# Optimization experiments

Hardware: AMD Instinct MI355X
Metric: run time of the kernel (lower is better)

Reference implementation:

```python
import jax, jax.numpy as jnp
from jax import lax
import numpy as np

B = 8; T = 64000
NFFT = 1024; HOP = 256
SC = 20; KS = 1024; PAD = 512
HEADS = 8; GH = 64; GO = 32
SPEC_DIM = 32 * (NFFT // 4) // 2   # 4096
NODE_DIM = SC + SPEC_DIM           # 4116
EPS = 1e-5
NEG_SLOPE = 0.2


def setup_inputs() -> dict:
    ks = jax.random.split(jax.random.key(0), 12)
    f32 = jnp.float32
    def rn(k, shp, s):
        return jax.random.normal(k, shp, dtype=f32) * s
    return {
        "x": jax.random.normal(ks[0], (B, 1, T), dtype=f32),
        "sinc_w": rn(ks[1], (SC, 1, KS), 0.03),
        "conv1_w": rn(ks[2], (32, 1, 3, 3), 0.1),
        "conv1_b": jnp.zeros((32,), f32),
        "bn1_g": jnp.ones((32,), f32),
        "bn1_b": jnp.zeros((32,), f32),
        "conv2_w": rn(ks[3], (32, 32, 3, 3), 0.06),
        "conv2_b": jnp.zeros((32,), f32),
        "bn2_g": jnp.ones((32,), f32),
        "bn2_b": jnp.zeros((32,), f32),
        "gat1_W": rn(ks[4], (NODE_DIM, HEADS * GH), 0.015),
        "gat1_asrc": rn(ks[5], (HEADS, GH), 0.1),
        "gat1_adst": rn(ks[6], (HEADS, GH), 0.1),
        "gat1_bias": jnp.zeros((HEADS * GH,), f32),
        "gat2_W": rn(ks[7], (HEADS * GH, GO), 0.04),
        "gat2_asrc": rn(ks[8], (1, GO), 0.1),
        "gat2_adst": rn(ks[9], (1, GO), 0.1),
        "gat2_bias": jnp.zeros((GO,), f32),
        "fc1_w": rn(ks[10], (GO, 128), 0.15),
        "fc1_b": jnp.zeros((128,), f32),
        "bnf_g": jnp.ones((128,), f32),
        "bnf_b": jnp.zeros((128,), f32),
        "fc2_w": rn(ks[11], (128, 2), 0.08),
        "fc2_b": jnp.zeros((2,), f32),
    }


def _bn2d_eval(z, g, b):
    # eval-mode BatchNorm2d with running_mean=0, running_var=1
    s = g / jnp.sqrt(1.0 + EPS)
    return z * s[None, :, None, None] + b[None, :, None, None]


def _conv2d(z, w, b):
    y = lax.conv_general_dilated(z, w, (1, 1), ((1, 1), (1, 1)),
                                 dimension_numbers=("NCHW", "OIHW", "NCHW"))
    return y + b[None, :, None, None]


def _gat_dense(hin, W, asrc, adst, bias, heads, fo, concat):
    # PyG GATConv on a fully-connected graph (add_self_loops=True default
    # => every node attends to all nodes including itself). Eval mode (no dropout).
    b, n, d = hin.shape
    h = jnp.einsum("bnd,dhf->bnhf", hin, W.reshape(d, heads, fo))
    s_src = jnp.einsum("bnhf,hf->bnh", h, asrc)   # alpha_j contribution
    s_dst = jnp.einsum("bnhf,hf->bnh", h, adst)   # alpha_i contribution
    e = jax.nn.leaky_relu(s_dst[:, :, None, :] + s_src[:, None, :, :], NEG_SLOPE)  # (b,i,j,h)
    a = jax.nn.softmax(e, axis=2)                 # softmax over sources j per dest i
    out = jnp.einsum("bijh,bjhf->bihf", a, h)
    out = out.reshape(b, n, heads * fo) if concat else out.mean(axis=2)
    return out + bias


def reference(x, sinc_w, conv1_w, conv1_b, bn1_g, bn1_b, conv2_w, conv2_b,
              bn2_g, bn2_b, gat1_W, gat1_asrc, gat1_adst, gat1_bias,
              gat2_W, gat2_asrc, gat2_adst, gat2_bias,
              fc1_w, fc1_b, bnf_g, bnf_b, fc2_w, fc2_b):
    b = x.shape[0]
    # --- sinc (band-pass) conv branch: conv1d k=1024, pad=512 ---
    sinc = lax.conv_general_dilated(x, sinc_w, (1,), ((PAD, PAD),),
                                    dimension_numbers=("NCH", "OIH", "NCH"))  # (b,20,T+1)
    Ls = (sinc.shape[-1] // 4) * 4
    sinc_feat = sinc[:, :, :Ls].reshape(b, SC, Ls // 4, 4).mean(-1)  # avg_pool1d(4)
    sinc_feat = jnp.transpose(sinc_feat, (0, 2, 1))                  # (b, Ls//4, 20)

    # --- STFT branch (torch.stft: center=True, reflect pad, rect window) ---
    xw = x[:, 0, :]
    xp = jnp.pad(xw, ((0, 0), (NFFT // 2, NFFT // 2)), mode="reflect")
    n_frames = 1 + T // HOP  # 251
    idx = np.arange(n_frames)[:, None] * HOP + np.arange(NFFT)
    frames = xp[:, idx]                                   # (b, 251, 1024)
    mag = jnp.abs(jnp.fft.rfft(frames, axis=-1))          # (b, 251, 513)
    logmag = jnp.log(mag + 1e-9)
    s = jnp.transpose(logmag, (0, 2, 1))[:, None]         # (b, 1, 513, 251)

    h = jax.nn.relu(_bn2d_eval(_conv2d(s, conv1_w, conv1_b), bn1_g, bn1_b))
    h = jax.nn.relu(_bn2d_eval(_conv2d(h, conv2_w, conv2_b), bn2_g, bn2_b))
    Fq = (h.shape[2] // 2) * 2
    Tt = (h.shape[3] // 2) * 2
    h = h[:, :, :Fq, :Tt].reshape(b, 32, Fq // 2, 2, Tt // 2, 2).max(axis=(3, 5))  # maxpool 2x2
    spec_feat = jnp.transpose(h, (0, 3, 1, 2)).reshape(b, -1, SPEC_DIM)  # (b, 250, 4096)

    n = min(sinc_feat.shape[1], spec_feat.shape[1])  # 250
    nodes = jnp.concatenate([sinc_feat[:, :n], spec_feat[:, :n]], axis=-1)  # (b,250,4116)

    g1 = jax.nn.relu(_gat_dense(nodes, gat1_W, gat1_asrc, gat1_adst, gat1_bias, HEADS, GH, True))
    g2 = _gat_dense(g1, gat2_W, gat2_asrc, gat2_adst, gat2_bias, 1, GO, False)
    emb = g2.mean(axis=1)  # (b, 32) graph-mean readout

    z = emb @ fc1_w + fc1_b
    z = jax.nn.relu(z * (bnf_g / jnp.sqrt(1.0 + EPS)) + bnf_b)  # eval BN1d
    out = z @ fc2_w + fc2_b
    return (out, emb)
```

## Files before the change

kernel.cpp:

```cpp
#include <hip/hip_runtime.h>
#include <hip/hip_bf16.h>
#include <math.h>

#define TB 8
#define TT 64000
#define NFRAMES 251
#define NROWS (TB*NFRAMES)
#define GROWS 2048
#define NBINS 513
#define NBPAD 576
#define NNODE 250
#define NODE_DIM 4116
#define KPAD 4128

typedef __attribute__((ext_vector_type(8))) short short8;
typedef __attribute__((ext_vector_type(4))) float floatx4;

static __device__ __forceinline__ unsigned short f2bf(float x) {
    __hip_bfloat16 h = __float2bfloat16(x);
    return *(unsigned short*)&h;
}
static __device__ __forceinline__ float bf2f(unsigned short u) {
    __hip_bfloat16 h = *(__hip_bfloat16*)&u;
    return __bfloat162float(h);
}

__global__ __launch_bounds__(256) void k_prep(
    const float* __restrict__ x, const float* __restrict__ sinc_w,
    const float* __restrict__ c2w, const float* __restrict__ g2bn,
    const float* __restrict__ c1w, const float* __restrict__ g1bn,
    const float* __restrict__ W,
    unsigned short* __restrict__ fh, unsigned short* __restrict__ fl,
    unsigned short* __restrict__ bch, unsigned short* __restrict__ bcl,
    unsigned short* __restrict__ bsh, unsigned short* __restrict__ bsl,
    unsigned short* __restrict__ wbt, unsigned short* __restrict__ Bp,
    unsigned short* __restrict__ Bc1,
    unsigned short* __restrict__ Wt, unsigned short* __restrict__ nodesb,
    unsigned short* __restrict__ h1t, unsigned short* __restrict__ h2t) {
    __shared__ unsigned short tile[64][65];
    int bi = blockIdx.x, tid = threadIdx.x;
    if (bi < 2048) {
        int idx = bi * 256 + tid;
        int row = idx >> 8, r = idx & 255;
        int b = row >> 8, j = row & 255;
        int u = j * 256 + r - 512;
        if (u < 0) u = -u;
        if (u >= TT) u = 2 * TT - 2 - u;
        float v = x[b * TT + u];
        unsigned short h = f2bf(v);
        fh[idx] = h;
        fl[idx] = f2bf(v - bf2f(h));
    } else if (bi < 2624) {
        int idx = (bi - 2048) * 256 + tid;
        int k = idx >> 8, r = idx & 255;
        float s = 0.f, c = 0.f;
        if (k < NBINS) {
            int mm = (k * r) & 1023;
            sincospif((float)mm * (1.0f / 512.0f), &s, &c);
        }
        unsigned short chv = f2bf(c), shv = f2bf(s);
        bch[idx] = chv; bcl[idx] = f2bf(c - bf2f(chv));
        bsh[idx] = shv; bsl[idx] = f2bf(s - bf2f(shv));
    } else if (bi < 3144) {
        int local = bi - 2624;
        int kt = local % 65, nt = local / 65;
        for (int idx = tid; idx < 4096; idx += 256) {
            int r = idx >> 6, c = idx & 63;
            int kp = kt * 64 + r;
            int k;
            if (kp < 20) k = kp;
            else if (kp < NODE_DIM) { int t = kp - 20; k = 20 + (t & 15) * 256 + (t >> 4); }
            else k = -1;
            float v = (k >= 0) ? W[k * 512 + nt * 64 + c] : 0.f;
            tile[r][c] = f2bf(v);
        }
        __syncthreads();
        for (int idx = tid; idx < 4096; idx += 256) {
            int nl = idx >> 6, kl = idx & 63;
            int k = kt * 64 + kl;
            if (k < KPAD)
                Wt[(size_t)(nt * 64 + nl) * KPAD + k] = tile[kl][nl];
        }
    } else if (bi < 3276) {
        int idx = (bi - 3144) * 256 + tid;
        if (idx < 32 * 1056) {
            int c = idx / 1056, m = idx - c * 1056;
            float s = 0.f;
            if (c < 20 && m < 1027) {
                #pragma unroll
                for (int d = 0; d < 4; d++) {
                    int k = m - d;
                    if (k >= 0 && k < 1024) s += sinc_w[c * 1024 + k];
                }
                s *= 0.25f;
            }
            wbt[idx] = f2bf(s);
        }
    } else if (bi < 3312) {
        int idx = (bi - 3276) * 256 + tid;
        if (idx < 9216) {
            int j = idx & 7, lane = (idx >> 3) & 63, ct = (idx >> 9) & 1, s = idx >> 10;
            int co = ct * 16 + (lane & 15);
            int ci = (lane >> 4) * 8 + j;
            float inv = rsqrtf(1.0f + 1e-5f);
            Bp[idx] = f2bf(c2w[co * 288 + ci * 9 + s] * (g2bn[co] * inv));
        }
    } else if (bi < 3508) {
        int idx = (bi - 3312) * 256 + tid;
        if (idx < 24000) {
            int row = idx / 12, c = idx - row * 12;
            nodesb[(size_t)row * KPAD + 4116 + c] = 0;
        } else if (idx < 48576) {
            int t = idx - 24000; int r = t / 6, c = t - r * 6;
            h1t[(size_t)r * 256 + 250 + c] = 0;
        } else if (idx < 50112) {
            int t = idx - 48576; int r = t / 6, c = t - r * 6;
            h2t[(size_t)r * 256 + 250 + c] = 0;
        }
    } else {
        int idx = (bi - 3508) * 256 + tid;
        if (idx < 1024) {
            int ch = idx >> 5, k = idx & 31;
            float inv = rsqrtf(1.0f + 1e-5f);
            int t; int typ;
            if (k < 8)       { t = k;      typ = 0; }
            else if (k < 16) { t = k - 8;  typ = 0; }
            else if (k < 24) { t = k - 16; typ = 1; }
            else if (k == 24 || k == 25) { t = 8; typ = 0; }
            else if (k == 26) { t = 8; typ = 1; }
            else { t = 0; typ = 2; }
            unsigned short outv = 0;
            if (typ != 2) {
                float wv = c1w[ch * 9 + t] * (g1bn[ch] * inv);
                unsigned short whi = f2bf(wv);
                outv = (typ == 0) ? whi : f2bf(wv - bf2f(whi));
            }
            Bc1[idx] = outv;
        }
    }
}

__global__ __launch_bounds__(256) void k_sincm(const float* __restrict__ x,
                                               const unsigned short* __restrict__ wbt,
                                               unsigned short* __restrict__ nodesb) {
    __shared__ __align__(16) unsigned short xs[1312];
    int ut = blockIdx.x, b = blockIdx.y;
    int tid = threadIdx.x;
    int base = 256 * ut - 512;
    for (int i = tid; i < 1312; i += 256) {
        int g = base + i;
        float v = (g >= 0 && g < TT) ? x[b * TT + g] : 0.f;
        xs[i] = f2bf(v);
    }
    __syncthreads();
    int w = tid >> 6, lane = tid & 63;
    int q = lane >> 4, col = lane & 15;
    floatx4 acc[2];
    acc[0] = acc[1] = (floatx4){0.f, 0.f, 0.f, 0.f};
    for (int K0 = 0; K0 < 1056; K0 += 32) {
        int off = 4 * (w * 16 + col) + K0 + q * 8;
        unsigned long long lo = *(const unsigned long long*)&xs[off];
        unsigned long long hi = *(const unsigned long long*)&xs[off + 4];
        union { unsigned long long u64[2]; short8 s8; } cv;
        cv.u64[0] = lo; cv.u64[1] = hi;
        short8 af = cv.s8;
        #pragma unroll
        for (int ni = 0; ni < 2; ni++) {
            short8 bf = *(const short8*)(wbt + (size_t)(ni * 16 + col) * 1056 + K0 + q * 8);
            acc[ni] = __builtin_amdgcn_mfma_f32_16x16x32_bf16(af, bf, acc[ni], 0, 0, 0);
        }
    }
    #pragma unroll
    for (int ni = 0; ni < 2; ni++)
        #pragma unroll
        for (int rr = 0; rr < 4; rr++) {
            int u = ut * 64 + w * 16 + q * 4 + rr;
            int c = ni * 16 + col;
            if (u < NNODE && c < 20)
                nodesb[(size_t)(b * NNODE + u) * KPAD + c] = f2bf(acc[ni][rr]);
        }
}

__global__ __launch_bounds__(256) void k_dft_mfma(const unsigned short* __restrict__ fh,
                                                  const unsigned short* __restrict__ fl,
                                                  const unsigned short* __restrict__ ch,
                                                  const unsigned short* __restrict__ cl,
                                                  const unsigned short* __restrict__ sh,
                                                  const unsigned short* __restrict__ sl,
                                                  float* __restrict__ GRo,
                                                  float* __restrict__ GIo) {
    __shared__ __align__(16) unsigned short Ah[32 * 40];
    __shared__ __align__(16) unsigned short Al[32 * 40];
    __shared__ __align__(16) unsigned short Bch[64 * 40];
    __shared__ __align__(16) unsigned short Bcl[64 * 40];
    __shared__ __align__(16) unsigned short Bsh[64 * 40];
    __shared__ __align__(16) unsigned short Bsl[64 * 40];
    int tid = threadIdx.x;
    int N0 = blockIdx.x * 64, M0 = blockIdx.y * 32;
    int br = tid >> 2, bc = (tid & 3) * 8;
    size_t boff = (size_t)(N0 + br) * 256 + bc;
    int ar = (tid & 127) >> 2, ac = (tid & 3) * 8;
    size_t aoff = (size_t)(M0 + ar) * 256 + ac;
    bool loA = tid < 128;
    int w = tid >> 6, lane = tid & 63;
    int q = lane >> 4, col = lane & 15;
    int mb = (w >> 1) * 16, nb = (w & 1) * 32;
    floatx4 aR[2], aI[2];
    aR[0] = aR[1] = aI[0] = aI[1] = (floatx4){0.f, 0.f, 0.f, 0.f};

    for (int K0 = 0; K0 < 256; K0 += 32) {
        if (loA) *(short8*)&Ah[ar * 40 + ac] = *(const short8*)(fh + aoff + K0);
        else     *(short8*)&Al[ar * 40 + ac] = *(const short8*)(fl + aoff + K0);
        *(short8*)&Bch[br * 40 + bc] = *(const short8*)(ch + boff + K0);
        *(short8*)&Bcl[br * 40 + bc] = *(const short8*)(cl + boff + K0);
        *(short8*)&Bsh[br * 40 + bc] = *(const short8*)(sh + boff + K0);
        *(short8*)&Bsl[br * 40 + bc] = *(const short8*)(sl + boff + K0);
        __syncthreads();
        short8 ahv = *(const short8*)&Ah[(mb + col) * 40 + q * 8];
        short8 alv = *(const short8*)&Al[(mb + col) * 40 + q * 8];
        #pragma unroll
        for (int ni = 0; ni < 2; ni++) {
            short8 chv = *(const short8*)&Bch[(nb + ni * 16 + col) * 40 + q * 8];
            short8 clv = *(const short8*)&Bcl[(nb + ni * 16 + col) * 40 + q * 8];
            short8 shv = *(const short8*)&Bsh[(nb + ni * 16 + col) * 40 + q * 8];
            short8 slv = *(const short8*)&Bsl[(nb + ni * 16 + col) * 40 + q * 8];
            aR[ni] = __builtin_amdgcn_mfma_f32_16x16x32_bf16(ahv, chv, aR[ni], 0, 0, 0);
            aR[ni] = __builtin_amdgcn_mfma_f32_16x16x32_bf16(ahv, clv, aR[ni], 0, 0, 0);
            aR[ni] = __builtin_amdgcn_mfma_f32_16x16x32_bf16(alv, chv, aR[ni], 0, 0, 0);
            aI[ni] = __builtin_amdgcn_mfma_f32_16x16x32_bf16(ahv, shv, aI[ni], 0, 0, 0);
            aI[ni] = __builtin_amdgcn_mfma_f32_16x16x32_bf16(ahv, slv, aI[ni], 0, 0, 0);
            aI[ni] = __builtin_amdgcn_mfma_f32_16x16x32_bf16(alv, shv, aI[ni], 0, 0, 0);
        }
        __syncthreads();
    }
    #pragma unroll
    for (int ni = 0; ni < 2; ni++)
        #pragma unroll
        for (int rr = 0; rr < 4; rr++) {
            int m = M0 + mb + q * 4 + rr;
            int bin = N0 + nb + ni * 16 + col;
            GRo[(size_t)m * NBPAD + bin] = aR[ni][rr];
            GIo[(size_t)m * NBPAD + bin] = aI[ni][rr];
        }
}

__global__ __launch_bounds__(256) void k_dftcomb(const float* __restrict__ GR,
                                                 const float* __restrict__ GI,
                                                 float* __restrict__ S0) {
    int idx = blockIdx.x * 256 + threadIdx.x;
    if (idx >= NROWS * NBINS) return;
    int mg = idx / NBINS, bin = idx - mg * NBINS;
    int b = mg / NFRAMES, i = mg - b * NFRAMES;
    size_t base = ((size_t)(b * 256 + i)) * NBPAD + bin;
    float gr0 = GR[base], gr1 = GR[base + NBPAD], gr2 = GR[base + 2 * NBPAD], gr3 = GR[base + 3 * NBPAD];
    float gs0 = GI[base], gs1 = GI[base + NBPAD], gs2 = GI[base + 2 * NBPAD], gs3 = GI[base + 3 * NBPAD];
    float fre, fim;
    switch (bin & 3) {
        case 0: fre = gr0 + gr1 + gr2 + gr3; fim = gs0 + gs1 + gs2 + gs3; break;
        case 1: fre = gr0 - gs1 - gr2 + gs3; fim = gs0 + gr1 - gs2 - gr3; break;
        case 2: fre = gr0 - gr1 + gr2 - gr3; fim = gs0 - gs1 + gs2 - gs3; break;
        default: fre = gr0 + gs1 - gr2 - gs3; fim = gs0 - gr1 - gs2 + gr3; break;
    }
    S0[(b * NBINS + bin) * NFRAMES + i] = logf(sqrtf(fmaf(fre, fre, fim * fim)) + 1e-9f);
}

#define O1STR 40
__global__ __launch_bounds__(256) void k_conv2f(const float* __restrict__ S0,
                                                const unsigned short* __restrict__ Bc1,
                                                const float* __restrict__ c1b,
                                                const float* __restrict__ g1bn,
                                                const float* __restrict__ b1bn,
                                                const unsigned short* __restrict__ Bp,
                                                const float* __restrict__ c2b,
                                                const float* __restrict__ g2bn,
                                                const float* __restrict__ b2bn,
                                                unsigned short* __restrict__ nodesb) {
    __shared__ __align__(16) unsigned short o1s[18 * 18 * O1STR];
    __shared__ float S0s[20][20];
    __shared__ float b1s[32];
    __shared__ float b2s[32];
    int tid = threadIdx.x;
    int b = blockIdx.z;
    int F0 = blockIdx.y * 8;
    int T0 = blockIdx.x * 8;
    float inv = rsqrtf(1.0f + 1e-5f);
    if (tid < 32) {
        b1s[tid] = c1b[tid] * (g1bn[tid] * inv) + b1bn[tid];
        b2s[tid] = c2b[tid] * (g2bn[tid] * inv) + b2bn[tid];
    }
    for (int i = tid; i < 400; i += 256) {
        int r = i / 20, c = i - r * 20;
        int rr = 2 * F0 - 2 + r, cc = 2 * T0 - 2 + c;
        float v = 0.f;
        if (rr >= 0 && rr < 513 && cc >= 0 && cc < 251)
            v = S0[((size_t)b * 513 + rr) * 251 + cc];
        S0s[r][c] = v;
    }
    __syncthreads();

    int lane = tid & 63, w = tid >> 6;
    int q = lane >> 4, col = lane & 15;

    {
        short8 bfr0 = *(const short8*)(Bc1 + (size_t)col * 32 + q * 8);
        short8 bfr1 = *(const short8*)(Bc1 + (size_t)(16 + col) * 32 + q * 8);
        for (int mt = w; mt < 21; mt += 4) {
            int p = mt * 16 + col;
            int pc = p < 324 ? p : 0;
            int pr = (pc * 228) >> 12;
            int pt = pc - pr * 18;
            float tv[9];
            #pragma unroll
            for (int di = 0; di < 3; di++)
                #pragma unroll
                for (int dj = 0; dj < 3; dj++)
                    tv[di * 3 + dj] = S0s[pr + di][pt + dj];
            unsigned short hu[9], lu[9];
            #pragma unroll
            for (int i = 0; i < 9; i++) {
                hu[i] = f2bf(tv[i]);
                lu[i] = f2bf(tv[i] - bf2f(hu[i]));
            }
            short8 af;
            if (q == 1) {
                af[0] = lu[0]; af[1] = lu[1]; af[2] = lu[2]; af[3] = lu[3];
                af[4] = lu[4]; af[5] = lu[5]; af[6] = lu[6]; af[7] = lu[7];
            } else if (q == 3) {
                af[0] = hu[8]; af[1] = lu[8]; af[2] = hu[8]; af[3] = 0;
                af[4] = 0; af[5] = 0; af[6] = 0; af[7] = 0;
            } else {
                af[0] = hu[0]; af[1] = hu[1]; af[2] = hu[2]; af[3] = hu[3];
                af[4] = hu[4]; af[5] = hu[5]; af[6] = hu[6]; af[7] = hu[7];
            }
            floatx4 c0 = (floatx4){0.f, 0.f, 0.f, 0.f};
            floatx4 c1 = (floatx4){0.f, 0.f, 0.f, 0.f};
            c0 = __builtin_amdgcn_mfma_f32_16x16x32_bf16(af, bfr0, c0, 0, 0, 0);
            c1 = __builtin_amdgcn_mfma_f32_16x16x32_bf16(af, bfr1, c1, 0, 0, 0);
            #pragma unroll
            for (int rr2 = 0; rr2 < 4; rr2++) {
                int pp = mt * 16 + q * 4 + rr2;
                if (pp < 324) {
                    int qr = (pp * 228) >> 12, qt = pp - qr * 18;
                    int r1 = 2 * F0 - 1 + qr, t1 = 2 * T0 - 1 + qt;
                    bool valid = (r1 >= 0 && r1 < 513 && t1 >= 0 && t1 < 251);
                    float v0 = fmaxf(c0[rr2] + b1s[col], 0.f);
                    float v1 = fmaxf(c1[rr2] + b1s[16 + col], 0.f);
                    o1s[pp * O1STR + col]      = valid ? f2bf(v0) : (unsigned short)0;
                    o1s[pp * O1STR + 16 + col] = valid ? f2bf(v1) : (unsigned short)0;
                }
            }
        }
    }
    __syncthreads();

    floatx4 acc[4][2];
    #pragma unroll
    for (int rt = 0; rt < 4; rt++)
        #pragma unroll
        for (int ct = 0; ct < 2; ct++)
            acc[rt][ct] = (floatx4){0.f, 0.f, 0.f, 0.f};

    #pragma unroll
    for (int s = 0; s < 9; s++) {
        const int di = s / 3, dj = s % 3;
        short8 bf0 = *(const short8*)&Bp[(s * 2 + 0) * 512 + lane * 8];
        short8 bf1 = *(const short8*)&Bp[(s * 2 + 1) * 512 + lane * 8];
        #pragma unroll
        for (int rt = 0; rt < 4; rt++) {
            short8 af = *(const short8*)&o1s[((w * 4 + rt + di) * 18 + (col + dj)) * O1STR + q * 8];
            acc[rt][0] = __builtin_amdgcn_mfma_f32_16x16x32_bf16(af, bf0, acc[rt][0], 0, 0, 0);
            acc[rt][1] = __builtin_amdgcn_mfma_f32_16x16x32_bf16(af, bf1, acc[rt][1], 0, 0, 0);
        }
    }
    __syncthreads();

    unsigned short* nb = o1s;
    #pragma unroll
    for (int ct = 0; ct < 2; ct++) {
        float bb = b2s[ct * 16 + col];
        #pragma unroll
        for (int fp2 = 0; fp2 < 2; fp2++)
            #pragma unroll
            for (int tc2 = 0; tc2 < 2; tc2++) {
                float m0 = fmaxf(
                    fmaxf(acc[2 * fp2][ct][2 * tc2], acc[2 * fp2][ct][2 * tc2 + 1]),
                    fmaxf(acc[2 * fp2 + 1][ct][2 * tc2], acc[2 * fp2 + 1][ct][2 * tc2 + 1]));
                float v = fmaxf(m0 + bb, 0.f);
                int nl = (2 * q + tc2) * 2 + ct;
                int fl = 2 * w + fp2;
                nb[nl * 136 + fl * 16 + col] = f2bf(v);
            }
    }
    __syncthreads();

    int nl = tid >> 4, part = tid & 15;
    int node_g = 2 * T0 + nl;
    if (node_g < NNODE) {
        unsigned short* dst = nodesb + (size_t)(b * NNODE + node_g) * KPAD + 20 + F0 * 16 + part * 8;
        *(short8*)(dst) = *(const short8*)&nb[nl * 136 + part * 8];
    }
}

__global__ __launch_bounds__(256) void k_gat1s(const unsigned short* __restrict__ A,
                                               const unsigned short* __restrict__ Bt,
                                               float* __restrict__ hpart) {
    __shared__ __align__(16) unsigned short As[64 * 40];
    __shared__ __align__(16) unsigned short Bs[64 * 40];
    int tid = threadIdx.x;
    int N0 = blockIdx.x * 64, M0 = blockIdx.y * 64;
    int kc = blockIdx.z;
    int ks = (kc == 0) ? 0 : (33 + 32 * (kc - 1));
    int ke = 33 + 32 * kc;
    if (kc == 0) ke = 33;
    int sr = tid >> 2, sc = (tid & 3) * 8;
    int w = tid >> 6, lane = tid & 63;
    int q = lane >> 4, col = lane & 15;
    int mb = (w >> 1) * 32, nb = (w & 1) * 32;
    floatx4 acc[2][2];
    acc[0][0] = acc[0][1] = acc[1][0] = acc[1][1] = (floatx4){0.f, 0.f, 0.f, 0.f};
    short8 z8 = {0, 0, 0, 0, 0, 0, 0, 0};
    int mA = M0 + sr;
    bool mv = mA < 2000;
    const unsigned short* pa = A + (size_t)mA * KPAD + sc;
    const unsigned short* pb = Bt + (size_t)(N0 + sr) * KPAD + sc;

    for (int kk = ks; kk < ke; kk++) {
        int K0 = kk * 32;
        short8 va = mv ? *(const short8*)(pa + K0) : z8;
        short8 vb = *(const short8*)(pb + K0);
        *(short8*)&As[sr * 40 + sc] = va;
        *(short8*)&Bs[sr * 40 + sc] = vb;
        __syncthreads();
        short8 a0 = *(const short8*)&As[(mb + col) * 40 + q * 8];
        short8 a1 = *(const short8*)&As[(mb + 16 + col) * 40 + q * 8];
        short8 b0 = *(const short8*)&Bs[(nb + col) * 40 + q * 8];
        short8 b1 = *(const short8*)&Bs[(nb + 16 + col) * 40 + q * 8];
        acc[0][0] = __builtin_amdgcn_mfma_f32_16x16x32_bf16(a0, b0, acc[0][0], 0, 0, 0);
        acc[0][1] = __builtin_amdgcn_mfma_f32_16x16x32_bf16(a0, b1, acc[0][1], 0, 0, 0);
        acc[1][0] = __builtin_amdgcn_mfma_f32_16x16x32_bf16(a1, b0, acc[1][0], 0, 0, 0);
        acc[1][1] = __builtin_amdgcn_mfma_f32_16x16x32_bf16(a1, b1, acc[1][1], 0, 0, 0);
        __syncthreads();
    }
    float* out = hpart + (size_t)kc * 1024000;
    #pragma unroll
    for (int mi = 0; mi < 2; mi++)
        #pragma unroll
        for (int ni = 0; ni < 2; ni++)
            #pragma unroll
            for (int rr = 0; rr < 4; rr++) {
                int m = M0 + mb + mi * 16 + q * 4 + rr;
                if (m < 2000)
                    out[m * 512 + N0 + nb + ni * 16 + col] = acc[mi][ni][rr];
            }
}

__global__ __launch_bounds__(256) void k_hred(const float* __restrict__ hpart,
                                              const float* __restrict__ asrc,
                                              const float* __restrict__ adst,
                                              unsigned short* __restrict__ h1t,
                                              float* __restrict__ ssrc,
                                              float* __restrict__ sdst) {
    int m = blockIdx.x;
    int tid = threadIdx.x;
    int n1 = tid, n2 = tid + 256;
    size_t base = (size_t)m * 512;
    float s1 = hpart[base + n1] + hpart[base + n1 + 1024000] +
               hpart[base + n1 + 2048000] + hpart[base + n1 + 3072000];
    float s2 = hpart[base + n2] + hpart[base + n2 + 1024000] +
               hpart[base + n2 + 2048000] + hpart[base + n2 + 3072000];
    int bb = m / NNODE, j = m - bb * NNODE;
    int hh1 = n1 >> 6, f1 = n1 & 63;
    int hh2 = n2 >> 6, f2 = n2 & 63;
    h1t[((size_t)((bb * 8 + hh1) * 64 + f1)) * 256 + j] = f2bf(s1);
    h1t[((size_t)((bb * 8 + hh2) * 64 + f2)) * 256 + j] = f2bf(s2);
    float ps1 = s1 * asrc[n1], pd1 = s1 * adst[n1];
    float ps2 = s2 * asrc[n2], pd2 = s2 * adst[n2];
    for (int off = 32; off > 0; off >>= 1) {
        ps1 += __shfl_down(ps1, off); pd1 += __shfl_down(pd1, off);
        ps2 += __shfl_down(ps2, off); pd2 += __shfl_down(pd2, off);
    }
    int lane = tid & 63, w = tid >> 6;
    if (lane == 0) {
        ssrc[m * 8 + w] = ps1;     sdst[m * 8 + w] = pd1;
        ssrc[m * 8 + 4 + w] = ps2; sdst[m * 8 + 4 + w] = pd2;
    }
}

__global__ __launch_bounds__(256) void k_attw(const float* __restrict__ ssrc,
                                              const float* __restrict__ sdst,
                                              unsigned short* __restrict__ Pn) {
    int bh = blockIdx.x;
    int b = bh >> 3, h = bh & 7;
    int tid = threadIdx.x;
    __shared__ float ss[NNODE];
    __shared__ float red[4];
    for (int j = tid; j < NNODE; j += 256) ss[j] = ssrc[(b * NNODE + j) * 8 + h];
    __syncthreads();
    float mv = (tid < NNODE) ? ss[tid] : -1e30f;
    for (int off = 32; off > 0; off >>= 1) mv = fmaxf(mv, __shfl_down(mv, off));
    if ((tid & 63) == 0) red[tid >> 6] = mv;
    __syncthreads();
    float smaxv = fmaxf(fmaxf(red[0], red[1]), fmaxf(red[2], red[3]));
    unsigned short* row = Pn + ((size_t)bh * 256 + tid) * 256;
    short8 z8 = {0, 0, 0, 0, 0, 0, 0, 0};
    if (tid >= NNODE) {
        #pragma unroll
        for (int j = 0; j < 256; j += 8) *(short8*)(row + j) = z8;
        return;
    }
    float d = sdst[(b * NNODE + tid) * 8 + h];
    float e0 = d + smaxv;
    float mx = e0 > 0.f ? e0 : 0.2f * e0;
    float den = 0.f;
    for (int j = 0; j < NNODE; j++) {
        float e = d + ss[j];
        e = e > 0.f ? e : 0.2f * e;
        den += __expf(e - mx);
    }
    float rden = 1.f / den;
    for (int j0 = 0; j0 < 256; j0 += 8) {
        unsigned short wv[8];
        #pragma unroll
        for (int jj = 0; jj < 8; jj++) {
            int j = j0 + jj;
            float wt = 0.f;
            if (j < NNODE) {
                float e = d + ss[j];
                e = e > 0.f ? e : 0.2f * e;
                wt = __expf(e - mx) * rden;
            }
            wv[jj] = f2bf(wt);
        }
        *(short8*)(row + j0) = *(const short8*)wv;
    }
}

__global__ __launch_bounds__(256) void k_attnv(const unsigned short* __restrict__ Pn,
                                               const unsigned short* __restrict__ h1t,
                                               const float* __restrict__ bias,
                                               float* __restrict__ g1) {
    int bh = blockIdx.x;
    int b = bh >> 3, h = bh & 7;
    int tid = threadIdx.x;
    int w = tid >> 6, lane = tid & 63;
    int q = lane >> 4, col = lane & 15;
    const unsigned short* Pb = Pn + (size_t)bh * 65536;
    const unsigned short* Hb = h1t + (size_t)bh * 16384;
    floatx4 acc[4][4];
    #pragma unroll
    for (int mi = 0; mi < 4; mi++)
        #pragma unroll
        for (int ni = 0; ni < 4; ni++)
            acc[mi][ni] = (floatx4){0.f, 0.f, 0.f, 0.f};
    for (int k0 = 0; k0 < 256; k0 += 32) {
        short8 af[4], bf[4];
        #pragma unroll
        for (int mi = 0; mi < 4; mi++)
            af[mi] = *(const short8*)(Pb + (size_t)((w * 4 + mi) * 16 + col) * 256 + k0 + q * 8);
        #pragma unroll
        for (int ni = 0; ni < 4; ni++)
            bf[ni] = *(const short8*)(Hb + (size_t)(ni * 16 + col) * 256 + k0 + q * 8);
        #pragma unroll
        for (int mi = 0; mi < 4; mi++)
            #pragma unroll
            for (int ni = 0; ni < 4; ni++)
                acc[mi][ni] = __builtin_amdgcn_mfma_f32_16x16x32_bf16(af[mi], bf[ni], acc[mi][ni], 0, 0, 0);
    }
    #pragma unroll
    for (int mi = 0; mi < 4; mi++)
        #pragma unroll
        for (int ni = 0; ni < 4; ni++)
            #pragma unroll
            for (int rr = 0; rr < 4; rr++) {
                int i = (w * 4 + mi) * 16 + q * 4 + rr;
                int f = ni * 16 + col;
                if (i < NNODE)
                    g1[(b * NNODE + i) * 512 + h * 64 + f] =
                        fmaxf(acc[mi][ni][rr] + bias[h * 64 + f], 0.f);
            }
}

__global__ __launch_bounds__(256) void k_h2(const float* __restrict__ g1,
                                            const float* __restrict__ W2,
                                            const float* __restrict__ a2src,
                                            const float* __restrict__ a2dst,
                                            unsigned short* __restrict__ h2t,
                                            float* __restrict__ s2src,
                                            float* __restrict__ s2dst) {
    int row = blockIdx.x * 4 + (threadIdx.x >> 6);
    if (row >= 2000) return;
    int lane = threadIdx.x & 63;
    int o = lane & 31, half = lane >> 5;
    const float* gr = &g1[row * 512 + half * 256];
    float acc = 0.f;
    for (int k = 0; k < 256; k++) acc = fmaf(gr[k], W2[(half * 256 + k) * 32 + o], acc);
    acc += __shfl_down(acc, 32);
    float ps = acc * a2src[o], pd = acc * a2dst[o];
    for (int off = 16; off > 0; off >>= 1) {
        ps += __shfl_down(ps, off, 32);
        pd += __shfl_down(pd, off, 32);
    }
    if (lane == 0) { s2src[row] = ps; s2dst[row] = pd; }
    if (lane < 32) {
        int b = row / NNODE, j = row - b * NNODE;
        h2t[((size_t)(b * 32 + o)) * 256 + j] = f2bf(acc);
    }
}

__global__ __launch_bounds__(256) void k_attw2(const float* __restrict__ s2src,
                                               const float* __restrict__ s2dst,
                                               unsigned short* __restrict__ P2n) {
    int b = blockIdx.x;
    int tid = threadIdx.x;
    __shared__ float ss[NNODE];
    __shared__ float red[4];
    for (int j = tid; j < NNODE; j += 256) ss[j] = s2src[b * NNODE + j];
    __syncthreads();
    float mv = (tid < NNODE) ? ss[tid] : -1e30f;
    for (int off = 32; off > 0; off >>= 1) mv = fmaxf(mv, __shfl_down(mv, off));
    if ((tid & 63) == 0) red[tid >> 6] = mv;
    __syncthreads();
    float smaxv = fmaxf(fmaxf(red[0], red[1]), fmaxf(red[2], red[3]));
    unsigned short* row = P2n + ((size_t)b * 256 + tid) * 256;
    short8 z8 = {0, 0, 0, 0, 0, 0, 0, 0};
    if (tid >= NNODE) {
        #pragma unroll
        for (int j = 0; j < 256; j += 8) *(short8*)(row + j) = z8;
        return;
    }
    float d = s2dst[b * NNODE + tid];
    float e0 = d + smaxv;
    float mx = e0 > 0.f ? e0 : 0.2f * e0;
    float den = 0.f;
    for (int j = 0; j < NNODE; j++) {
        float e = d + ss[j];
        e = e > 0.f ? e : 0.2f * e;
        den += __expf(e - mx);
    }
    float rden = 1.f / den;
    for (int j0 = 0; j0 < 256; j0 += 8) {
        unsigned short wv[8];
        #pragma unroll
        for (int jj = 0; jj < 8; jj++) {
            int j = j0 + jj;
            float wt = 0.f;
            if (j < NNODE) {
                float e = d + ss[j];
                e = e > 0.f ? e : 0.2f * e;
                wt = __expf(e - mx) * rden;
            }
            wv[jj] = f2bf(wt);
        }
        *(short8*)(row + j0) = *(const short8*)wv;
    }
}

__global__ __launch_bounds__(256) void k_attnv2(const unsigned short* __restrict__ P2n,
                                                const unsigned short* __restrict__ h2t,
                                                const float* __restrict__ bias2,
                                                float* __restrict__ g2) {
    int b = blockIdx.x;
    int tid = threadIdx.x;
    int w = tid >> 6, lane = tid & 63;
    int q = lane >> 4, col = lane & 15;
    const unsigned short* Pb = P2n + (size_t)b * 65536;
    const unsigned short* Hb = h2t + (size_t)b * 8192;
    floatx4 acc[4][2];
    #pragma unroll
    for (int mi = 0; mi < 4; mi++)
        #pragma unroll
        for (int ni = 0; ni < 2; ni++)
            acc[mi][ni] = (floatx4){0.f, 0.f, 0.f, 0.f};
    for (int k0 = 0; k0 < 256; k0 += 32) {
        short8 af[4], bf[2];
        #pragma unroll
        for (int mi = 0; mi < 4; mi++)
            af[mi] = *(const short8*)(Pb + (size_t)((w * 4 + mi) * 16 + col) * 256 + k0 + q * 8);
        #pragma unroll
        for (int ni = 0; ni < 2; ni++)
            bf[ni] = *(const short8*)(Hb + (size_t)(ni * 16 + col) * 256 + k0 + q * 8);
        #pragma unroll
        for (int mi = 0; mi < 4; mi++)
            #pragma unroll
            for (int ni = 0; ni < 2; ni++)
                acc[mi][ni] = __builtin_amdgcn_mfma_f32_16x16x32_bf16(af[mi], bf[ni], acc[mi][ni], 0, 0, 0);
    }
    #pragma unroll
    for (int mi = 0; mi < 4; mi++)
        #pragma unroll
        for (int ni = 0; ni < 2; ni++)
            #pragma unroll
            for (int rr = 0; rr < 4; rr++) {
                int i = (w * 4 + mi) * 16 + q * 4 + rr;
                int f = ni * 16 + col;
                if (i < NNODE)
                    g2[(b * NNODE + i) * 32 + f] = acc[mi][ni][rr] + bias2[f];
            }
}

__global__ __launch_bounds__(256) void k_fc(const float* __restrict__ g2,
                                            const float* __restrict__ fc1w,
                                            const float* __restrict__ fc1b,
                                            const float* __restrict__ bnfg,
                                            const float* __restrict__ bnfb,
                                            const float* __restrict__ fc2w,
                                            const float* __restrict__ fc2b,
                                            float* __restrict__ dout) {
    __shared__ float es[256];
    __shared__ float zs[1024];
    int tid = threadIdx.x;
    {
        int b = tid >> 5, f = tid & 31;
        float s = 0.f;
        #pragma unroll 5
        for (int i = 0; i < NNODE; i++) s += g2[((size_t)(b * NNODE + i)) * 32 + f];
        s *= (1.0f / 250.0f);
        es[tid] = s;
        dout[16 + tid] = s;
    }
    __syncthreads();
    float inv = rsqrtf(1.0f + 1e-5f);
    #pragma unroll
    for (int rep = 0; rep < 4; rep++) {
        int idx = tid + rep * 256;
        int b = idx >> 7, j = idx & 127;
        float a = fc1b[j];
        #pragma unroll
        for (int k = 0; k < 32; k++) a = fmaf(es[b * 32 + k], fc1w[k * 128 + j], a);
        a = a * (bnfg[j] * inv) + bnfb[j];
        zs[idx] = fmaxf(a, 0.f);
    }
    __syncthreads();
    if (tid < 16) {
        int b = tid >> 1, o = tid & 1;
        float a = fc2b[o];
        for (int k = 0; k < 128; k++) a = fmaf(zs[b * 128 + k], fc2w[k * 2 + o], a);
        dout[b * 2 + o] = a;
    }
}

extern "C" void kernel_launch(void* const* d_in, const int* in_sizes, int n_in,
                              void* d_out, int out_size, void* d_ws, size_t ws_size,
                              hipStream_t stream) {
    (void)in_sizes; (void)n_in; (void)out_size; (void)ws_size;
    const float* x       = (const float*)d_in[0];
    const float* sinc_w  = (const float*)d_in[1];
    const float* conv1_w = (const float*)d_in[2];
    const float* conv1_b = (const float*)d_in[3];
    const float* bn1_g   = (const float*)d_in[4];
    const float* bn1_b   = (const float*)d_in[5];
    const float* conv2_w = (const float*)d_in[6];
    const float* conv2_b = (const float*)d_in[7];
    const float* bn2_g   = (const float*)d_in[8];
    const float* bn2_b   = (const float*)d_in[9];
    const float* gat1_W  = (const float*)d_in[10];
    const float* gat1_as = (const float*)d_in[11];
    const float* gat1_ad = (const float*)d_in[12];
    const float* gat1_bi = (const float*)d_in[13];
    const float* gat2_W  = (const float*)d_in[14];
    const float* gat2_as = (const float*)d_in[15];
    const float* gat2_ad = (const float*)d_in[16];
    const float* gat2_bi = (const float*)d_in[17];
    const float* fc1_w   = (const float*)d_in[18];
    const float* fc1_b   = (const float*)d_in[19];
    const float* bnf_g   = (const float*)d_in[20];
    const float* bnf_b   = (const float*)d_in[21];
    const float* fc2_w   = (const float*)d_in[22];
    const float* fc2_b   = (const float*)d_in[23];
    float* dout = (float*)d_out;

    unsigned short* fh  = (unsigned short*)d_ws;
    unsigned short* fl  = fh + (size_t)GROWS * 256;
    unsigned short* bch = fl + (size_t)GROWS * 256;
    unsigned short* bcl = bch + (size_t)NBPAD * 256;
    unsigned short* bsh = bcl + (size_t)NBPAD * 256;
    unsigned short* bsl = bsh + (size_t)NBPAD * 256;
    float* GRb = (float*)(bsl + (size_t)NBPAD * 256);
    float* GIb = GRb + (size_t)GROWS * NBPAD;
    float* S0  = GIb + (size_t)GROWS * NBPAD;
    unsigned short* wbt = (unsigned short*)(S0 + 1030104);
    unsigned short* bpk = wbt + 32 * 1056;
    unsigned short* Bc1 = bpk + 9216;
    unsigned short* Wt  = Bc1 + 1024;
    unsigned short* nodesb = Wt + (size_t)512 * KPAD;
    unsigned short* Pn  = nodesb + (size_t)2000 * KPAD;
    unsigned short* h1t = Pn + (size_t)64 * 256 * 256;
    unsigned short* h2t = h1t + (size_t)64 * 64 * 256;
    unsigned short* P2n = h2t + (size_t)8 * 32 * 256;
    float* hpart = (float*)(P2n + (size_t)8 * 256 * 256);
    float* ssrc1 = hpart + 4 * 1024000;
    float* sdst1 = ssrc1 + 16000;
    float* g1    = sdst1 + 16000;
    float* s2src = g1 + 1024000;
    float* s2dst = s2src + 2000;
    float* g2    = s2dst + 2000;

    hipLaunchKernelGGL(k_prep, dim3(3512), dim3(256), 0, stream,
                       x, sinc_w, conv2_w, bn2_g, conv1_w, bn1_g, gat1_W,
                       fh, fl, bch, bcl, bsh, bsl, wbt, bpk, Bc1, Wt, nodesb, h1t, h2t);
    hipLaunchKernelGGL(k_dft_mfma, dim3(9, 64), dim3(256), 0, stream,
                       fh, fl, bch, bcl, bsh, bsl, GRb, GIb);
    hipLaunchKernelGGL(k_dftcomb, dim3((NROWS * NBINS + 255) / 256), dim3(256), 0, stream,
                       GRb, GIb, S0);
    hipLaunchKernelGGL(k_sincm, dim3(4, 8), dim3(256), 0, stream, x, wbt, nodesb);
    hipLaunchKernelGGL(k_conv2f, dim3(16, 32, 8), dim3(256), 0, stream,
                       S0, Bc1, conv1_b, bn1_g, bn1_b, bpk, conv2_b, bn2_g, bn2_b, nodesb);
    hipLaunchKernelGGL(k_gat1s, dim3(8, 32, 4), dim3(256), 0, stream, nodesb, Wt, hpart);
    hipLaunchKernelGGL(k_hred, dim3(2000), dim3(256), 0, stream,
                       hpart, gat1_as, gat1_ad, h1t, ssrc1, sdst1);
    hipLaunchKernelGGL(k_attw, dim3(64), dim3(256), 0, stream, ssrc1, sdst1, Pn);
    hipLaunchKernelGGL(k_attnv, dim3(64), dim3(256), 0, stream, Pn, h1t, gat1_bi, g1);
    hipLaunchKernelGGL(k_h2, dim3(500), dim3(256), 0, stream,
                       g1, gat2_W, gat2_as, gat2_ad, h2t, s2src, s2dst);
    hipLaunchKernelGGL(k_attw2, dim3(8), dim3(256), 0, stream, s2src, s2dst, P2n);
    hipLaunchKernelGGL(k_attnv2, dim3(8), dim3(256), 0, stream, P2n, h2t, gat2_bi, g2);
    hipLaunchKernelGGL(k_fc, dim3(1), dim3(256), 0, stream,
                       g2, fc1_w, fc1_b, bnf_g, bnf_b, fc2_w, fc2_b, dout);
}
```

Measured before the change: 343.2 us.

## Fuse GAT attention-weight softmax into attention-value MFMA kernels via shared memory

Merges the softmax weight computation and the attention-times-values MFMA matmul for both GAT layers into single kernels. The bf16 probability matrix now stays in padded LDS instead of round-tripping through global memory, which also removes two launches. Layer 1 is split into two row-halves per batch-head (128 blocks) to keep parallelism. The cost is that only half the threads compute softmax rows in layer 1, and the large LDS footprint in layer 2 (about 135KB) may limit occupancy.

```diff
diff --git a/kernel.cpp b/kernel.cpp
--- a/kernel.cpp
+++ b/kernel.cpp
@@ -486,14 +486,18 @@
     }
 }
 
-__global__ __launch_bounds__(256) void k_attw(const float* __restrict__ ssrc,
+#define PSTR 264
+__global__ __launch_bounds__(256) void k_att1(const float* __restrict__ ssrc,
                                               const float* __restrict__ sdst,
-                                              unsigned short* __restrict__ Pn) {
-    int bh = blockIdx.x;
+                                              const unsigned short* __restrict__ h1t,
+                                              const float* __restrict__ bias,
+                                              float* __restrict__ g1) {
+    __shared__ __align__(16) unsigned short Ps[128 * PSTR];
+    __shared__ float ss[NNODE];
+    __shared__ float red[4];
+    int mhalf = blockIdx.x, bh = blockIdx.y;
     int b = bh >> 3, h = bh & 7;
     int tid = threadIdx.x;
-    __shared__ float ss[NNODE];
-    __shared__ float red[4];
     for (int j = tid; j < NNODE; j += 256) ss[j] = ssrc[(b * NNODE + j) * 8 + h];
     __syncthreads();
     float mv = (tid < NNODE) ? ss[tid] : -1e30f;
@@ -501,78 +505,72 @@
     if ((tid & 63) == 0) red[tid >> 6] = mv;
     __syncthreads();
     float smaxv = fmaxf(fmaxf(red[0], red[1]), fmaxf(red[2], red[3]));
-    unsigned short* row = Pn + ((size_t)bh * 256 + tid) * 256;
-    short8 z8 = {0, 0, 0, 0, 0, 0, 0, 0};
-    if (tid >= NNODE) {
-        #pragma unroll
-        for (int j = 0; j < 256; j += 8) *(short8*)(row + j) = z8;
-        return;
-    }
-    float d = sdst[(b * NNODE + tid) * 8 + h];
-    float e0 = d + smaxv;
-    float mx = e0 > 0.f ? e0 : 0.2f * e0;
-    float den = 0.f;
-    for (int j = 0; j < NNODE; j++) {
-        float e = d + ss[j];
-        e = e > 0.f ? e : 0.2f * e;
-        den += __expf(e - mx);
-    }
-    float rden = 1.f / den;
-    for (int j0 = 0; j0 < 256; j0 += 8) {
-        unsigned short wv[8];
-        #pragma unroll
-        for (int jj = 0; jj < 8; jj++) {
-            int j = j0 + jj;
-            float wt = 0.f;
-            if (j < NNODE) {
+    if (tid < 128) {
+        unsigned short* row = Ps + tid * PSTR;
+        int row_g = mhalf * 128 + tid;
+        short8 z8 = {0, 0, 0, 0, 0, 0, 0, 0};
+        if (row_g >= NNODE) {
+            #pragma unroll
+            for (int j = 0; j < 256; j += 8) *(short8*)(row + j) = z8;
+        } else {
+            float d = sdst[(b * NNODE + row_g) * 8 + h];
+            float e0 = d + smaxv;
+            float mx = e0 > 0.f ? e0 : 0.2f * e0;
+            float den = 0.f;
+            for (int j = 0; j < NNODE; j++) {
                 float e = d + ss[j];
                 e = e > 0.f ? e : 0.2f * e;
-                wt = __expf(e - mx) * rden;
-            }
-            wv[jj] = f2bf(wt);
-        }
-        *(short8*)(row + j0) = *(const short8*)wv;
-    }
-}
-
-__global__ __launch_bounds__(256) void k_attnv(const unsigned short* __restrict__ Pn,
-                                               const unsigned short* __restrict__ h1t,
-                                               const float* __restrict__ bias,
-                                               float* __restrict__ g1) {
-    int bh = blockIdx.x;
-    int b = bh >> 3, h = bh & 7;
-    int tid = threadIdx.x;
+                den += __expf(e - mx);
+            }
+            float rden = 1.f / den;
+            for (int j0 = 0; j0 < 256; j0 += 8) {
+                unsigned short wv[8];
+                #pragma unroll
+                for (int jj = 0; jj < 8; jj++) {
+                    int j = j0 + jj;
+                    float wt = 0.f;
+                    if (j < NNODE) {
+                        float e = d + ss[j];
+                        e = e > 0.f ? e : 0.2f * e;
+                        wt = __expf(e - mx) * rden;
+                    }
+                    wv[jj] = f2bf(wt);
+                }
+                *(short8*)(row + j0) = *(const short8*)wv;
+            }
+        }
+    }
+    __syncthreads();
     int w = tid >> 6, lane = tid & 63;
     int q = lane >> 4, col = lane & 15;
-    const unsigned short* Pb = Pn + (size_t)bh * 65536;
     const unsigned short* Hb = h1t + (size_t)bh * 16384;
-    floatx4 acc[4][4];
-    #pragma unroll
-    for (int mi = 0; mi < 4; mi++)
+    floatx4 acc[2][4];
+    #pragma unroll
+    for (int mi = 0; mi < 2; mi++)
         #pragma unroll
         for (int ni = 0; ni < 4; ni++)
             acc[mi][ni] = (floatx4){0.f, 0.f, 0.f, 0.f};
     for (int k0 = 0; k0 < 256; k0 += 32) {
-        short8 af[4], bf[4];
-        #pragma unroll
-        for (int mi = 0; mi < 4; mi++)
-            af[mi] = *(const short8*)(Pb + (size_t)((w * 4 + mi) * 16 + col) * 256 + k0 + q * 8);
+        short8 af[2], bf[4];
+        #pragma unroll
+        for (int mi = 0; mi < 2; mi++)
+            af[mi] = *(const short8*)&Ps[((w * 2 + mi) * 16 + col) * PSTR + k0 + q * 8];
         #pragma unroll
         for (int ni = 0; ni < 4; ni++)
             bf[ni] = *(const short8*)(Hb + (size_t)(ni * 16 + col) * 256 + k0 + q * 8);
         #pragma unroll
-        for (int mi = 0; mi < 4; mi++)
+        for (int mi = 0; mi < 2; mi++)
             #pragma unroll
             for (int ni = 0; ni < 4; ni++)
                 acc[mi][ni] = __builtin_amdgcn_mfma_f32_16x16x32_bf16(af[mi], bf[ni], acc[mi][ni], 0, 0, 0);
     }
     #pragma unroll
-    for (int mi = 0; mi < 4; mi++)
+    for (int mi = 0; mi < 2; mi++)
         #pragma unroll
         for (int ni = 0; ni < 4; ni++)
             #pragma unroll
             for (int rr = 0; rr < 4; rr++) {
-                int i = (w * 4 + mi) * 16 + q * 4 + rr;
+                int i = mhalf * 128 + (w * 2 + mi) * 16 + q * 4 + rr;
                 int f = ni * 16 + col;
                 if (i < NNODE)
                     g1[(b * NNODE + i) * 512 + h * 64 + f] =
@@ -607,13 +605,16 @@
     }
 }
 
-__global__ __launch_bounds__(256) void k_attw2(const float* __restrict__ s2src,
-                                               const float* __restrict__ s2dst,
-                                               unsigned short* __restrict__ P2n) {
+__global__ __launch_bounds__(256) void k_att2(const float* __restrict__ s2src,
+                                              const float* __restrict__ s2dst,
+                                              const unsigned short* __restrict__ h2t,
+                                              const float* __restrict__ bias2,
+                                              float* __restrict__ g2) {
+    __shared__ __align__(16) unsigned short Ps[256 * PSTR];
+    __shared__ float ss[NNODE];
+    __shared__ float red[4];
     int b = blockIdx.x;
     int tid = threadIdx.x;
-    __shared__ float ss[NNODE];
-    __shared__ float red[4];
     for (int j = tid; j < NNODE; j += 256) ss[j] = s2src[b * NNODE + j];
     __syncthreads();
     float mv = (tid < NNODE) ? ss[tid] : -1e30f;
@@ -621,49 +622,43 @@
     if ((tid & 63) == 0) red[tid >> 6] = mv;
     __syncthreads();
     float smaxv = fmaxf(fmaxf(red[0], red[1]), fmaxf(red[2], red[3]));
-    unsigned short* row = P2n + ((size_t)b * 256 + tid) * 256;
-    short8 z8 = {0, 0, 0, 0, 0, 0, 0, 0};
-    if (tid >= NNODE) {
-        #pragma unroll
-        for (int j = 0; j < 256; j += 8) *(short8*)(row + j) = z8;
-        return;
-    }
-    float d = s2dst[b * NNODE + tid];
-    float e0 = d + smaxv;
-    float mx = e0 > 0.f ? e0 : 0.2f * e0;
-    float den = 0.f;
-    for (int j = 0; j < NNODE; j++) {
-        float e = d + ss[j];
-        e = e > 0.f ? e : 0.2f * e;
-        den += __expf(e - mx);
-    }
-    float rden = 1.f / den;
-    for (int j0 = 0; j0 < 256; j0 += 8) {
-        unsigned short wv[8];
-        #pragma unroll
-        for (int jj = 0; jj < 8; jj++) {
-            int j = j0 + jj;
-            float wt = 0.f;
-            if (j < NNODE) {
+    {
+        unsigned short* row = Ps + tid * PSTR;
+        short8 z8 = {0, 0, 0, 0, 0, 0, 0, 0};
+        if (tid >= NNODE) {
+            #pragma unroll
+            for (int j = 0; j < 256; j += 8) *(short8*)(row + j) = z8;
+        } else {
+            float d = s2dst[b * NNODE + tid];
+            float e0 = d + smaxv;
+            float mx = e0 > 0.f ? e0 : 0.2f * e0;
+            float den = 0.f;
+            for (int j = 0; j < NNODE; j++) {
                 float e = d + ss[j];
                 e = e > 0.f ? e : 0.2f * e;
-                wt = __expf(e - mx) * rden;
-            }
-            wv[jj] = f2bf(wt);
-        }
-        *(short8*)(row + j0) = *(const short8*)wv;
-    }
-}
-
-__global__ __launch_bounds__(256) void k_attnv2(const unsigned short* __restrict__ P2n,
-                                                const unsigned short* __restrict__ h2t,
-                                                const float* __restrict__ bias2,
-                                                float* __restrict__ g2) {
-    int b = blockIdx.x;
-    int tid = threadIdx.x;
+                den += __expf(e - mx);
+            }
+            float rden = 1.f / den;
+            for (int j0 = 0; j0 < 256; j0 += 8) {
+                unsigned short wv[8];
+                #pragma unroll
+                for (int jj = 0; jj < 8; jj++) {
+                    int j = j0 + jj;
+                    float wt = 0.f;
+                    if (j < NNODE) {
+                        float e = d + ss[j];
+                        e = e > 0.f ? e : 0.2f * e;
+                        wt = __expf(e - mx) * rden;
+                    }
+                    wv[jj] = f2bf(wt);
+                }
+                *(short8*)(row + j0) = *(const short8*)wv;
+            }
+        }
+    }
+    __syncthreads();
     int w = tid >> 6, lane = tid & 63;
     int q = lane >> 4, col = lane & 15;
-    const unsigned short* Pb = P2n + (size_t)b * 65536;
     const unsigned short* Hb = h2t + (size_t)b * 8192;
     floatx4 acc[4][2];
     #pragma unroll
@@ -675,7 +670,7 @@
         short8 af[4], bf[2];
         #pragma unroll
         for (int mi = 0; mi < 4; mi++)
-            af[mi] = *(const short8*)(Pb + (size_t)((w * 4 + mi) * 16 + col) * 256 + k0 + q * 8);
+            af[mi] = *(const short8*)&Ps[((w * 4 + mi) * 16 + col) * PSTR + k0 + q * 8];
         #pragma unroll
         for (int ni = 0; ni < 2; ni++)
             bf[ni] = *(const short8*)(Hb + (size_t)(ni * 16 + col) * 256 + k0 + q * 8);
@@ -808,12 +803,12 @@
     hipLaunchKernelGGL(k_gat1s, dim3(8, 32, 4), dim3(256), 0, stream, nodesb, Wt, hpart);
     hipLaunchKernelGGL(k_hred, dim3(2000), dim3(256), 0, stream,
                        hpart, gat1_as, gat1_ad, h1t, ssrc1, sdst1);
-    hipLaunchKernelGGL(k_attw, dim3(64), dim3(256), 0, stream, ssrc1, sdst1, Pn);
-    hipLaunchKernelGGL(k_attnv, dim3(64), dim3(256), 0, stream, Pn, h1t, gat1_bi, g1);
+    hipLaunchKernelGGL(k_att1, dim3(2, 64), dim3(256), 0, stream,
+                       ssrc1, sdst1, h1t, gat1_bi, g1);
     hipLaunchKernelGGL(k_h2, dim3(500), dim3(256), 0, stream,
                        g1, gat2_W, gat2_as, gat2_ad, h2t, s2src, s2dst);
-    hipLaunchKernelGGL(k_attw2, dim3(8), dim3(256), 0, stream, s2src, s2dst, P2n);
-    hipLaunchKernelGGL(k_attnv2, dim3(8), dim3(256), 0, stream, P2n, h2t, gat2_bi, g2);
+    hipLaunchKernelGGL(k_att2, dim3(8), dim3(256), 0, stream,
+                       s2src, s2dst, h2t, gat2_bi, g2);
     hipLaunchKernelGGL(k_fc, dim3(1), dim3(256), 0, stream,
                        g2, fc1_w, fc1_b, bnf_g, bnf_b, fc2_w, fc2_b, dout);
 }
```

Measured after the change: 327.5 us. 1.05x faster.
